# Optimization experiments

Hardware: AMD Instinct MI355X
Metric: run time of the kernel (lower is better)

The kernel has to match this reference:

```python
import jax, jax.numpy as jnp
import numpy as np

NQ, N, C = 8192, 32768, 128


def setup_inputs() -> dict:
    key = jax.random.key(0)
    k1, k2, k3 = jax.random.split(key, 3)
    return {
        "query_pos": jax.random.normal(k1, (NQ, 3), dtype=jnp.float32),
        "neural_feat": jax.random.normal(k2, (N, C), dtype=jnp.float32),
        "neural_pos": jax.random.normal(k3, (N, 3), dtype=jnp.float32),
        "knn": 64,
    }


def _cdist(a, b):
    # Euclidean pairwise distances via the (|a|^2 + |b|^2 - 2ab) expansion.
    a2 = jnp.sum(a * a, axis=-1, keepdims=True)          # [N',1]
    b2 = jnp.sum(b * b, axis=-1)                          # [N]
    d2 = a2 + b2[None, :] - 2.0 * (a @ b.T)               # [N',N]
    return jnp.sqrt(jnp.maximum(d2, 1e-12))


def reference(query_pos, neural_feat, neural_pos, knn):
    dists = _cdist(query_pos, neural_pos)                 # [N',N]
    # torch.topk(largest=False, sorted=True) == top_k of negated dists.
    neg_vals, closest_ind = jax.lax.top_k(-dists, knn)    # [N',k]
    closest_dists = -neg_vals                             # ascending
    closest_feat = neural_feat[closest_ind]               # [N',k,C] gather
    inv_dist = 1.0 / (closest_dists + 1e-5)               # [N',k]
    retrieved_feat = jnp.sum(closest_feat * inv_dist[..., None], axis=1)  # [N',C]
    return retrieved_feat
```

## Files before the change

### kernel.cpp

```cpp
#include <hip/hip_runtime.h>
#include <math.h>

#define NQ    8192
#define NPTS  32768
#define KNN   64
#define CAP   256
#define RCAP  256
#define PG    64
#define PNC   (PG*PG*PG)
#define PCELL 0.15f
#define PGINV (PG / 9.6f)
#define QG    32
#define QNC   (QG*QG*QG)
#define QGINV (QG / 9.6f)
#define GLO   (-4.8f)
#define NBLK  2048
#define TGT   (110.0f / 32768.0f)
#define PCHUNKS (PNC / 1024)
#define QCHUNKS (QNC / 1024)

__device__ __forceinline__ unsigned key_of(float f) {
  unsigned u = __float_as_uint(f);
  return (u & 0x80000000u) ? ~u : (u | 0x80000000u);
}
__device__ __forceinline__ float val_of(unsigned k) {
  unsigned u = (k & 0x80000000u) ? (k & 0x7fffffffu) : ~k;
  return __uint_as_float(u);
}
__device__ __forceinline__ int mbcnt64(unsigned long long m) {
  return __builtin_amdgcn_mbcnt_hi((unsigned)(m >> 32),
         __builtin_amdgcn_mbcnt_lo((unsigned)m, 0));
}
__device__ __forceinline__ float rflf(float x) {
  return __int_as_float(__builtin_amdgcn_readfirstlane(__float_as_int(x)));
}
__device__ __forceinline__ int rfli(int x) { return __builtin_amdgcn_readfirstlane(x); }

__device__ __forceinline__ float norm_cdf(float x) { return 0.5f * erfcf(-x * 0.70710678f); }
__device__ __forceinline__ float ball_mass(float mu, float r) {
  float a = r - mu, b = r + mu;
  float e = __expf(-0.5f * b * b) - __expf(-0.5f * a * a);
  return e / (mu * 2.50662827f) + norm_cdf(a) - norm_cdf(-mu) + norm_cdf(b) - norm_cdf(mu);
}

__device__ __forceinline__ int cidxP(float v) {
  int i = (int)floorf((v - GLO) * PGINV);
  return min(max(i, 0), PG - 1);
}
__device__ __forceinline__ int cidxQ(float v) {
  int i = (int)floorf((v - GLO) * QGINV);
  return min(max(i, 0), QG - 1);
}


__global__ __launch_bounds__(256) void hist_tau_kernel(
    const float* __restrict__ pos, const float* __restrict__ qpos,
    int* __restrict__ pcnt, int* __restrict__ qcnt, float* __restrict__ tau) {
  const int gid = blockIdx.x * 256 + threadIdx.x;
  const float x = pos[gid * 3 + 0], y = pos[gid * 3 + 1], z = pos[gid * 3 + 2];
  atomicAdd(&pcnt[(cidxP(z) * PG + cidxP(y)) * PG + cidxP(x)], 1);
  if (gid < NQ) {
    const float qx = qpos[gid * 3 + 0], qy = qpos[gid * 3 + 1], qz = qpos[gid * 3 + 2];
    atomicAdd(&qcnt[(cidxQ(qz) * QG + cidxQ(qy)) * QG + cidxQ(qx)], 1);
    const float b = qx * qx + qy * qy + qz * qz;
    const float mu = fmaxf(sqrtf(b), 0.05f);
    float lo = 0.f, hi = mu + 8.f;
    for (int i = 0; i < 16; ++i) {
      const float r = 0.5f * (lo + hi);
      if (ball_mass(mu, r) < TGT) lo = r; else hi = r;
    }
    tau[gid] = hi * hi;
  }
}

__global__ __launch_bounds__(256) void scan_kernel(
    int* __restrict__ pcnt, int* __restrict__ qcnt, int* __restrict__ cellStart,
    int* __restrict__ ppub, int* __restrict__ qpub) {
  __shared__ int aux[256];
  __shared__ int off[256];
  const int t = threadIdx.x;
  const bool isP = (blockIdx.x < PCHUNKS);
  const int cb = isP ? blockIdx.x : (blockIdx.x - PCHUNKS);
  int* src = isP ? pcnt : qcnt;
  int* pub = isP ? ppub : qpub;
  const int base = cb * 1024 + t * 4;
  const int4 q = ((const int4*)(src + base))[0];
  aux[t] = q.x + q.y + q.z + q.w;
  __syncthreads();
  for (int o = 1; o < 256; o <<= 1) {
    const int u = (t >= o) ? aux[t - o] : 0;
    __syncthreads();
    aux[t] += u;
    __syncthreads();
  }
  if (t == 0) atomicExch(&pub[cb], aux[255] + 1);
  int v = 0;
  if (t < cb) {
    while ((v = atomicOr(&pub[t], 0)) == 0) { }
    v -= 1;
  }
  off[t] = v;
  __syncthreads();
  for (int o = 128; o; o >>= 1) {
    if (t < o) off[t] += off[t + o];
    __syncthreads();
  }
  const int chunkOff = off[0];
  int run = (t ? aux[t - 1] : 0) + chunkOff;
  int4 w;
  w.x = run; run += q.x;
  w.y = run; run += q.y;
  w.z = run; run += q.z;
  w.w = run; run += q.w;
  if (isP) {
    ((int4*)(cellStart + base))[0] = w;
    ((int4*)(pcnt + base))[0] = w;
    if (cb == PCHUNKS - 1 && t == 255) cellStart[PNC] = NPTS;
  } else {
    ((int4*)(qcnt + base))[0] = w;
  }
}

__global__ __launch_bounds__(256) void scatter_kernel(
    const float* __restrict__ pos, const float* __restrict__ qpos,
    int* __restrict__ pcur, int* __restrict__ qcur, const float* __restrict__ tau,
    float4* __restrict__ pts, float4* __restrict__ qp, float* __restrict__ qtau) {
  const int gid = blockIdx.x * 256 + threadIdx.x;
  const float x = pos[gid * 3 + 0], y = pos[gid * 3 + 1], z = pos[gid * 3 + 2];
  const int c = (cidxP(z) * PG + cidxP(y)) * PG + cidxP(x);
  const int slot = atomicAdd(&pcur[c], 1);
  pts[slot] = make_float4(x, y, z, __int_as_float(gid));
  if (gid < NQ) {
    const float a = qpos[gid * 3 + 0], b = qpos[gid * 3 + 1], d = qpos[gid * 3 + 2];
    const int qc = (cidxQ(d) * QG + cidxQ(b)) * QG + cidxQ(a);
    const int qs = atomicAdd(&qcur[qc], 1);
    qp[qs] = make_float4(a, b, d, __int_as_float(gid));
    qtau[qs] = tau[gid];
  }
}


__global__ __launch_bounds__(256, 8) void knn_main(
    const float* __restrict__ feat, const int* __restrict__ cellStart,
    const float4* __restrict__ pts, const float4* __restrict__ qp,
    const float* __restrict__ qtau, float* __restrict__ out) {

  __shared__ uint2 sCand[4][CAP];
  __shared__ uint2 sSel[4][KNN];
  __shared__ int   sRC[4][RCAP];
  __shared__ int   sAdj[4][RCAP];

  const int tid = threadIdx.x, lane = tid & 63, wv = tid >> 6;
  const int bid = blockIdx.x;
  const int swz = (bid & 7) * (NBLK / 8) + (bid >> 3);
  const int sq  = swz * 4 + wv;

  const float4 Q = qp[sq];
  const float qx = rflf(Q.x), qy = rflf(Q.y), qz = rflf(Q.z);
  const int orig = rfli(__float_as_int(Q.w));
  const float bq = qx * qx + qy * qy + qz * qz;
  const float nx = -2.f * qx, ny = -2.f * qy, nz = -2.f * qz;
  float r2 = rflf(qtau[sq]);
  float tlo = 0.f, thi = -1.f;
  int cnt = 0;

  for (int attempt = 0; attempt < 12; ++attempt) {
    const float r = sqrtf(r2);
    const float tq = r2 - bq;
    const int iy0 = cidxP(qy - r), iy1 = cidxP(qy + r);
    const int iz0 = cidxP(qz - r), iz1 = cidxP(qz + r);
    const int nyw  = iy1 - iy0 + 1;
    const int nrow = nyw * (iz1 - iz0 + 1);
    cnt = 0;
    int nbuf = 0, tot = 0;

    auto probe_pt = [&](int pi, bool have) {
      const float4 P = pts[have ? pi : 0];
      const float n = P.x * P.x + P.y * P.y + P.z * P.z;
      const float d = fmaf(P.z, nz, fmaf(P.y, ny, fmaf(P.x, nx, n)));
      const bool hh = have && (d < tq);
      const unsigned long long m = __ballot(hh);
      if (m) {
        const int p = cnt + mbcnt64(m);
        if (hh && p < CAP)
          sCand[wv][p] = make_uint2(key_of(d + bq), __float_as_uint(P.w));
        cnt += (int)__popcll(m);
      }
    };

    auto drain = [&]() {
      if (nbuf == 0) return;
      if (nbuf <= 64) {
        const int rcv = (lane < nbuf) ? sRC[wv][lane] : 0x7FFFFFFF;
        const int adv = (lane < nbuf) ? sAdj[wv][lane] : 0;
        for (int b = 0; b < tot; b += 64) {
          const int fi = b + lane;
          const bool have = fi < tot;
          int ro = 0;
          #pragma unroll
          for (int st = 32; st; st >>= 1) {
            const int nr = ro + st;
            const int probe = __shfl(rcv, min(nr, nbuf) - 1);
            if (nr <= nbuf && probe <= fi) ro = nr;
          }
          const int pi = fi + __shfl(adv, min(ro, nbuf - 1));
          probe_pt(pi, have);
        }
      } else {
        for (int b = 0; b < tot; b += 64) {
          const int fi = b + lane;
          const bool have = fi < tot;
          int ro = 0;
          #pragma unroll
          for (int st = 128; st; st >>= 1) {
            const int nr = ro + st;
            if (nr <= nbuf && sRC[wv][nr - 1] <= fi) ro = nr;
          }
          const int pi = fi + sAdj[wv][min(ro, nbuf - 1)];
          probe_pt(pi, have);
        }
      }
      nbuf = 0; tot = 0;
    };

    auto issue = [&](int rcb, int& sR, int& eR, bool& vd) {
      vd = false; sR = 0; eR = 0;
      const int myrow = rcb + lane;
      if (myrow < nrow) {
        const int dz = myrow / nyw;
        const int dy = myrow - dz * nyw;
        const int giy = iy0 + dy, giz = iz0 + dz;
        const float ylo = GLO + giy * PCELL;
        const float zlo = GLO + giz * PCELL;
        const float dyv = fmaxf(0.f, fmaxf(ylo - qy, qy - (ylo + PCELL)));
        const float dzv = fmaxf(0.f, fmaxf(zlo - qz, qz - (zlo + PCELL)));
        const float dd = dyv * dyv + dzv * dzv;
        if (dd < r2) {
          const float hx = sqrtf(r2 - dd);
          const int jx0 = cidxP(qx - hx), jx1 = cidxP(qx + hx);
          const int rb = (giz * PG + giy) * PG;
          sR = cellStart[rb + jx0];
          eR = cellStart[rb + jx1 + 1];
          vd = true;
        }
      }
    };

    int sR0 = 0, eR0 = 0; bool v0 = false;
    issue(0, sR0, eR0, v0);
    for (int rc = 0; rc < nrow; rc += 64) {
      int sR1 = 0, eR1 = 0; bool v1 = false;
      if (rc + 64 < nrow) issue(rc + 64, sR1, eR1, v1);
      const int c = v0 ? (eR0 - sR0) : 0;
      const int s = v0 ? sR0 : 0;
      int cum = c;
      #pragma unroll
      for (int off = 1; off < 64; off <<= 1) {
        const int u = __shfl_up(cum, off);
        if (lane >= off) cum += u;
      }
      const unsigned long long act = __ballot(c > 0);
      const int slot = nbuf + mbcnt64(act);
      if (c > 0) {
        sRC[wv][slot]  = tot + cum;
        sAdj[wv][slot] = s - (tot + cum - c);
      }
      nbuf += (int)__popcll(act);
      tot  += __shfl(cum, 63);
      if (nbuf > RCAP - 64) drain();
      sR0 = sR1; eR0 = eR1; v0 = v1;
    }
    drain();

    if (cnt >= KNN && cnt <= CAP) break;
    if (cnt < KNN) { tlo = r2; r2 = (thi < 0.f) ? r2 * 3.f : 0.5f * (r2 + thi); }
    else           { thi = r2; r2 = 0.5f * (tlo + r2); }
  }

  {
    const int mm = min(cnt, CAP);
    unsigned k[4], id[4];
    #pragma unroll
    for (int s = 0; s < 4; ++s) {
      const int g2 = s * 64 + lane;
      uint2 kv = make_uint2(0xFFFFFFFFu, 0u);
      if (g2 < mm) kv = sCand[wv][g2];
      k[s] = kv.x; id[s] = kv.y;
    }
    unsigned blo = 0x80000000u, bhi = 0xFFFFFFFFu;
    for (int it = 0; it < 32; ++it) {
      const unsigned mid = blo + ((bhi - blo) >> 1);
      const int c = (int)(__popcll(__ballot(k[0] <= mid)) + __popcll(__ballot(k[1] <= mid)) +
                          __popcll(__ballot(k[2] <= mid)) + __popcll(__ballot(k[3] <= mid)));
      if (c >= KNN) bhi = mid; else blo = mid + 1;
    }
    const unsigned K = blo;

    int fill = 0;
    #pragma unroll
    for (int s = 0; s < 4; ++s) {
      const bool lt = k[s] < K;
      const unsigned long long msk = __ballot(lt);
      if (msk) {
        const int p = fill + mbcnt64(msk);
        if (lt) { const float dv = val_of(k[s]);
                  const float w_ = 1.f / (sqrtf(fmaxf(dv, 1e-12f)) + 1e-5f);
                  sSel[wv][p] = make_uint2(id[s], __float_as_uint(w_)); }
        fill += (int)__popcll(msk);
      }
    }
    #pragma unroll
    for (int s = 0; s < 4; ++s) {
      const bool eq = (k[s] == K);
      const unsigned long long msk = __ballot(eq);
      if (msk) {
        const int p = fill + mbcnt64(msk);
        if (eq && p < KNN) { const float dv = val_of(k[s]);
                             const float w_ = 1.f / (sqrtf(fmaxf(dv, 1e-12f)) + 1e-5f);
                             sSel[wv][p] = make_uint2(id[s], __float_as_uint(w_)); }
        fill += (int)__popcll(msk);
      }
    }
  }

  {
    const int half = lane >> 5;
    const int col  = lane & 31;
    float4 acc = make_float4(0.f, 0.f, 0.f, 0.f);
    #pragma unroll 4
    for (int j = 0; j < KNN; j += 2) {
      const uint2 pr = sSel[wv][j + half];
      const float w = __uint_as_float(pr.y);
      const float4 f4 = *(const float4*)(feat + ((size_t)pr.x << 7) + (col << 2));
      acc.x = fmaf(w, f4.x, acc.x);
      acc.y = fmaf(w, f4.y, acc.y);
      acc.z = fmaf(w, f4.z, acc.z);
      acc.w = fmaf(w, f4.w, acc.w);
    }
    acc.x += __shfl_xor(acc.x, 32);
    acc.y += __shfl_xor(acc.y, 32);
    acc.z += __shfl_xor(acc.z, 32);
    acc.w += __shfl_xor(acc.w, 32);
    if (lane < 32)
      *(float4*)(out + ((size_t)orig << 7) + (col << 2)) = acc;
  }
}

extern "C" void kernel_launch(void* const* d_in, const int* in_sizes, int n_in,
                              void* d_out, int out_size, void* d_ws, size_t ws_size,
                              hipStream_t stream) {
  const float* qpos = (const float*)d_in[0];
  const float* feat = (const float*)d_in[1];
  const float* pos  = (const float*)d_in[2];
  float* out = (float*)d_out;

  char* ws = (char*)d_ws;
  int*    pcnt      = (int*)(ws);
  int*    qcnt      = (int*)(ws + (1024 << 10));
  int*    ppub      = (int*)(ws + (1152 << 10));
  int*    qpub      = (int*)(ws + (1153 << 10));
  int*    cellStart = (int*)(ws + (1156 << 10));
  float*  tau       = (float*)(ws + (2188 << 10));
  float4* pts       = (float4*)(ws + (2220 << 10));
  float4* qp        = (float4*)(ws + (2732 << 10));
  float*  qtau      = (float*)(ws + (2860 << 10));

  hipMemsetAsync(ws, 0, 1154 << 10, stream);
  hist_tau_kernel<<<dim3(NPTS / 256),        dim3(256), 0, stream>>>(pos, qpos, pcnt, qcnt, tau);
  scan_kernel    <<<dim3(PCHUNKS + QCHUNKS), dim3(256), 0, stream>>>(pcnt, qcnt, cellStart, ppub, qpub);
  scatter_kernel <<<dim3(NPTS / 256),        dim3(256), 0, stream>>>(pos, qpos, pcnt, qcnt, tau, pts, qp, qtau);
  knn_main       <<<dim3(NBLK),              dim3(256), 0, stream>>>(feat, cellStart, pts, qp, qtau, out);
}
```

Measured before the change: 116.0 us.

## Fuse scan and scatter kernels with a device-wide done counter; trim tau bisection

Merges the prefix-scan and scatter launches into one kernel. Scatter blocks preload their positions, then spin on a global done counter until all scan blocks have published their offsets. This removes one kernel launch and its gap, at the cost of relying on scan blocks (lower block indices) being scheduled before scatter blocks spin. The tau bisection also drops from 16 to 12 iterations, which makes the search radius slightly less precise.

```diff
diff --git a/kernel.cpp b/kernel.cpp
--- a/kernel.cpp
+++ b/kernel.cpp
@@ -18,6 +18,8 @@
 #define TGT   (110.0f / 32768.0f)
 #define PCHUNKS (PNC / 1024)
 #define QCHUNKS (QNC / 1024)
+#define SCANB  (PCHUNKS + QCHUNKS)
+#define SCATB  (NPTS / 256)
 
 __device__ __forceinline__ unsigned key_of(float f) {
   unsigned u = __float_as_uint(f);
@@ -65,7 +67,7 @@
     const float b = qx * qx + qy * qy + qz * qz;
     const float mu = fmaxf(sqrtf(b), 0.05f);
     float lo = 0.f, hi = mu + 8.f;
-    for (int i = 0; i < 16; ++i) {
+    for (int i = 0; i < 12; ++i) {
       const float r = 0.5f * (lo + hi);
       if (ball_mass(mu, r) < TGT) lo = r; else hi = r;
     }
@@ -73,69 +75,82 @@
   }
 }
 
-__global__ __launch_bounds__(256) void scan_kernel(
+__global__ __launch_bounds__(256) void scan_scatter_kernel(
+    const float* __restrict__ pos, const float* __restrict__ qpos,
     int* __restrict__ pcnt, int* __restrict__ qcnt, int* __restrict__ cellStart,
-    int* __restrict__ ppub, int* __restrict__ qpub) {
+    int* __restrict__ ppub, int* __restrict__ qpub, int* __restrict__ done,
+    const float* __restrict__ tau, float4* __restrict__ pts,
+    float4* __restrict__ qp, float* __restrict__ qtau) {
   __shared__ int aux[256];
   __shared__ int off[256];
   const int t = threadIdx.x;
-  const bool isP = (blockIdx.x < PCHUNKS);
-  const int cb = isP ? blockIdx.x : (blockIdx.x - PCHUNKS);
-  int* src = isP ? pcnt : qcnt;
-  int* pub = isP ? ppub : qpub;
-  const int base = cb * 1024 + t * 4;
-  const int4 q = ((const int4*)(src + base))[0];
-  aux[t] = q.x + q.y + q.z + q.w;
-  __syncthreads();
-  for (int o = 1; o < 256; o <<= 1) {
-    const int u = (t >= o) ? aux[t - o] : 0;
+
+  if (blockIdx.x < SCANB) {
+    const bool isP = (blockIdx.x < PCHUNKS);
+    const int cb = isP ? blockIdx.x : (blockIdx.x - PCHUNKS);
+    int* src = isP ? pcnt : qcnt;
+    int* pub = isP ? ppub : qpub;
+    const int base = cb * 1024 + t * 4;
+    const int4 q = ((const int4*)(src + base))[0];
+    aux[t] = q.x + q.y + q.z + q.w;
     __syncthreads();
-    aux[t] += u;
+    for (int o = 1; o < 256; o <<= 1) {
+      const int u = (t >= o) ? aux[t - o] : 0;
+      __syncthreads();
+      aux[t] += u;
+      __syncthreads();
+    }
+    if (t == 0) atomicExch(&pub[cb], aux[255] + 1);
+    int v = 0;
+    if (t < cb) {
+      while ((v = atomicOr(&pub[t], 0)) == 0) { }
+      v -= 1;
+    }
+    off[t] = v;
     __syncthreads();
-  }
-  if (t == 0) atomicExch(&pub[cb], aux[255] + 1);
-  int v = 0;
-  if (t < cb) {
-    while ((v = atomicOr(&pub[t], 0)) == 0) { }
-    v -= 1;
-  }
-  off[t] = v;
-  __syncthreads();
-  for (int o = 128; o; o >>= 1) {
-    if (t < o) off[t] += off[t + o];
+    for (int o = 128; o; o >>= 1) {
+      if (t < o) off[t] += off[t + o];
+      __syncthreads();
+    }
+    const int chunkOff = off[0];
+    int run = (t ? aux[t - 1] : 0) + chunkOff;
+    int4 w;
+    w.x = run; run += q.x;
+    w.y = run; run += q.y;
+    w.z = run; run += q.z;
+    w.w = run; run += q.w;
+    if (isP) {
+      ((int4*)(cellStart + base))[0] = w;
+      ((int4*)(pcnt + base))[0] = w;
+      if (cb == PCHUNKS - 1 && t == 255) cellStart[PNC] = NPTS;
+    } else {
+      ((int4*)(qcnt + base))[0] = w;
+    }
+    __threadfence();
     __syncthreads();
-  }
-  const int chunkOff = off[0];
-  int run = (t ? aux[t - 1] : 0) + chunkOff;
-  int4 w;
-  w.x = run; run += q.x;
-  w.y = run; run += q.y;
-  w.z = run; run += q.z;
-  w.w = run; run += q.w;
-  if (isP) {
-    ((int4*)(cellStart + base))[0] = w;
-    ((int4*)(pcnt + base))[0] = w;
-    if (cb == PCHUNKS - 1 && t == 255) cellStart[PNC] = NPTS;
+    if (t == 0) atomicAdd(done, 1);
   } else {
-    ((int4*)(qcnt + base))[0] = w;
-  }
-}
-
-__global__ __launch_bounds__(256) void scatter_kernel(
-    const float* __restrict__ pos, const float* __restrict__ qpos,
-    int* __restrict__ pcur, int* __restrict__ qcur, const float* __restrict__ tau,
-    float4* __restrict__ pts, float4* __restrict__ qp, float* __restrict__ qtau) {
-  const int gid = blockIdx.x * 256 + threadIdx.x;
-  const float x = pos[gid * 3 + 0], y = pos[gid * 3 + 1], z = pos[gid * 3 + 2];
-  const int c = (cidxP(z) * PG + cidxP(y)) * PG + cidxP(x);
-  const int slot = atomicAdd(&pcur[c], 1);
-  pts[slot] = make_float4(x, y, z, __int_as_float(gid));
-  if (gid < NQ) {
-    const float a = qpos[gid * 3 + 0], b = qpos[gid * 3 + 1], d = qpos[gid * 3 + 2];
-    const int qc = (cidxQ(d) * QG + cidxQ(b)) * QG + cidxQ(a);
-    const int qs = atomicAdd(&qcur[qc], 1);
-    qp[qs] = make_float4(a, b, d, __int_as_float(gid));
-    qtau[qs] = tau[gid];
+    const int gid = (blockIdx.x - SCANB) * 256 + t;
+    const float x = pos[gid * 3 + 0], y = pos[gid * 3 + 1], z = pos[gid * 3 + 2];
+    const int c = (cidxP(z) * PG + cidxP(y)) * PG + cidxP(x);
+    float a = 0.f, b = 0.f, d = 0.f, tv = 0.f; int qc = 0;
+    if (gid < NQ) {
+      a = qpos[gid * 3 + 0]; b = qpos[gid * 3 + 1]; d = qpos[gid * 3 + 2];
+      qc = (cidxQ(d) * QG + cidxQ(b)) * QG + cidxQ(a);
+      tv = tau[gid];
+    }
+    if (t == 0) {
+      while (atomicOr(done, 0) < SCANB) __builtin_amdgcn_s_sleep(8);
+    }
+    __syncthreads();
+    __threadfence();
+    const int slot = atomicAdd(&pcnt[c], 1);
+    pts[slot] = make_float4(x, y, z, __int_as_float(gid));
+    if (gid < NQ) {
+      const int qs = atomicAdd(&qcnt[qc], 1);
+      qp[qs] = make_float4(a, b, d, __int_as_float(gid));
+      qtau[qs] = tv;
+    }
   }
 }
 
@@ -359,6 +374,7 @@
   int*    qcnt      = (int*)(ws + (1024 << 10));
   int*    ppub      = (int*)(ws + (1152 << 10));
   int*    qpub      = (int*)(ws + (1153 << 10));
+  int*    done      = (int*)(ws + (1153 << 10) + 128);
   int*    cellStart = (int*)(ws + (1156 << 10));
   float*  tau       = (float*)(ws + (2188 << 10));
   float4* pts       = (float4*)(ws + (2220 << 10));
@@ -366,8 +382,8 @@
   float*  qtau      = (float*)(ws + (2860 << 10));
 
   hipMemsetAsync(ws, 0, 1154 << 10, stream);
-  hist_tau_kernel<<<dim3(NPTS / 256),        dim3(256), 0, stream>>>(pos, qpos, pcnt, qcnt, tau);
-  scan_kernel    <<<dim3(PCHUNKS + QCHUNKS), dim3(256), 0, stream>>>(pcnt, qcnt, cellStart, ppub, qpub);
-  scatter_kernel <<<dim3(NPTS / 256),        dim3(256), 0, stream>>>(pos, qpos, pcnt, qcnt, tau, pts, qp, qtau);
-  knn_main       <<<dim3(NBLK),              dim3(256), 0, stream>>>(feat, cellStart, pts, qp, qtau, out);
-}
+  hist_tau_kernel   <<<dim3(NPTS / 256),   dim3(256), 0, stream>>>(pos, qpos, pcnt, qcnt, tau);
+  scan_scatter_kernel<<<dim3(SCANB + SCATB), dim3(256), 0, stream>>>(
+      pos, qpos, pcnt, qcnt, cellStart, ppub, qpub, done, tau, pts, qp, qtau);
+  knn_main          <<<dim3(NBLK),         dim3(256), 0, stream>>>(feat, cellStart, pts, qp, qtau, out);
+}
```

Result: slower. 153.1 us (+31.9%).
